# Performance work log

Hardware: AMD Instinct MI355X
Metric: run time of the kernel (lower is better)

## Reference

```python
import jax, jax.numpy as jnp
import numpy as np

H = 4      # SSM / attn heads (d_model/headdim = 256/64)
WIN = 4    # attention window over bands


def _ln(x, g, b):
    m = jnp.mean(x, -1, keepdims=True)
    v = jnp.mean((x - m) ** 2, -1, keepdims=True)
    return (x - m) * jax.lax.rsqrt(v + 1e-5) * g + b


def setup_inputs() -> dict:
    key = jax.random.key(0)
    ks = jax.random.split(key, 24)
    def rn(i, shape, s=0.05):
        return jax.random.normal(ks[i], shape, jnp.float32) * s
    B, T, K, D = 2, 256, 8, 256
    return {
        "z": rn(0, (B, T, K, D), 1.0),
        "ln1_g": jnp.ones((D,), jnp.float32), "ln1_b": jnp.zeros((D,), jnp.float32),
        "Wx": rn(1, (D, D)), "conv_w": rn(2, (D, 4), 0.3), "Wz": rn(3, (D, D)),
        "Wb": rn(4, (D, H * 128)), "Wc": rn(5, (D, H * 128)), "Wdt": rn(6, (D, H)),
        "dt_bias": rn(7, (H,), 0.5), "A_log": rn(8, (H,), 0.5), "theta": rn(9, (H,), 1.0),
        "D_skip": rn(10, (H,), 1.0), "mimo_U": rn(11, (H, H), 0.5), "mimo_V": rn(12, (H, H), 0.5),
        "Wout": rn(13, (D, D)),
        "ln2_g": jnp.ones((D,), jnp.float32), "ln2_b": jnp.zeros((D,), jnp.float32),
        "attn_in_w": rn(14, (3 * D, D)), "attn_in_b": rn(15, (3 * D,), 0.02),
        "attn_out_w": rn(16, (D, D)), "attn_out_b": jnp.zeros((D,), jnp.float32),
        "ln3_g": jnp.ones((D,), jnp.float32), "ln3_b": jnp.zeros((D,), jnp.float32),
        "Wg": rn(17, (D, 4 * D)), "Wu": rn(18, (D, 4 * D)), "Wd": rn(19, (4 * D, D)),
    }


def _forward(z, ln1_g, ln1_b, Wx, conv_w, Wz, Wb, Wc, Wdt, dt_bias, A_log, theta,
             D_skip, mimo_U, mimo_V, Wout, ln2_g, ln2_b, attn_in_w, attn_in_b,
             attn_out_w, attn_out_b, ln3_g, ln3_b, Wg, Wu, Wd):
    B, T, K, D = z.shape
    P = D // H
    N = Wb.shape[1] // H
    # ---------- (a) intra-band Mamba3 (complex MIMO selective scan) ----------
    u = _ln(z, ln1_g, ln1_b)
    u = jnp.transpose(u, (0, 2, 1, 3)).reshape(B * K, T, D)   # [BK,T,D]
    x = u @ Wx
    # causal depthwise conv1d, kernel 4
    xp = jnp.pad(x, ((0, 0), (3, 0), (0, 0)))
    x = sum(xp[:, k:k + T, :] * conv_w[:, k] for k in range(4))
    x = jax.nn.silu(x)
    xh = x.reshape(B * K, T, H, P)
    Bm = (u @ Wb).reshape(B * K, T, H, N)
    Cm = (u @ Wc).reshape(B * K, T, H, N)
    Mmix = mimo_U @ mimo_V.T                                  # rank-r cross-head coupling
    Bm = jnp.einsum('hg,btgn->bthn', Mmix, Bm)
    dt = jax.nn.softplus(u @ Wdt + dt_bias)                   # [BK,T,H]
    A = -jnp.exp(A_log)                                       # stable real decay
    mag = jnp.exp(dt * A)
    ph = dt * theta                                           # harmonic rotation
    ar, ai = mag * jnp.cos(ph), mag * jnp.sin(ph)
    xs = tuple(jnp.moveaxis(t, 1, 0) for t in (xh, Bm, Cm, dt, ar, ai))
    h0 = jnp.zeros((B * K, H, N, P), x.dtype)

    def step(carry, s):
        h_re, h_im = carry
        xt, bt, ct, dtt, art, ait = s
        dBx = (dtt[:, :, None, None] * bt[:, :, :, None]) * xt[:, :, None, :]
        nr = art[:, :, None, None] * h_re - ait[:, :, None, None] * h_im + dBx
        ni = art[:, :, None, None] * h_im + ait[:, :, None, None] * h_re
        return (nr, ni), jnp.einsum('bhn,bhnp->bhp', ct, nr)   # Re(C . h)

    _, ys = jax.lax.scan(step, (h0, h0), xs)                  # ys: [T,BK,H,P]
    y = jnp.moveaxis(ys, 0, 1) + D_skip[None, None, :, None] * xh
    y = y.reshape(B * K, T, D) * jax.nn.silu(u @ Wz)
    y = y @ Wout
    z = z + jnp.transpose(y.reshape(B, K, T, D), (0, 2, 1, 3))
    # ---------- (b) inter-band windowed attention ----------
    zn = _ln(z, ln2_g, ln2_b).reshape(B * T, K, D)
    qkv = zn @ attn_in_w.T + attn_in_b
    q, k_, v = jnp.split(qkv, 3, axis=-1)
    hd = D // H
    def hs(t):
        return t.reshape(B * T, K // WIN, WIN, H, hd).transpose(0, 1, 3, 2, 4)
    q, k_, v = hs(q), hs(k_), hs(v)
    s = jnp.einsum('mwhqd,mwhkd->mwhqk', q, k_) * jnp.float32(1.0 / np.sqrt(hd))
    a = jax.nn.softmax(s, axis=-1)
    o = jnp.einsum('mwhqk,mwhkd->mwhqd', a, v).transpose(0, 1, 3, 2, 4).reshape(B * T, K, D)
    z = z + (o @ attn_out_w.T + attn_out_b).reshape(B, T, K, D)
    # ---------- (c) SwiGLU FFN ----------
    zf = _ln(z, ln3_g, ln3_b)
    z = z + (jax.nn.silu(zf @ Wg) * (zf @ Wu)) @ Wd
    return z


def reference(z, ln1_g, ln1_b, Wx, conv_w, Wz, Wb, Wc, Wdt, dt_bias, A_log, theta,
              D_skip, mimo_U, mimo_V, Wout, ln2_g, ln2_b, attn_in_w, attn_in_b,
              attn_out_w, attn_out_b, ln3_g, ln3_b, Wg, Wu, Wd):
    return _forward(z, ln1_g, ln1_b, Wx, conv_w, Wz, Wb, Wc, Wdt, dt_bias, A_log,
                    theta, D_skip, mimo_U, mimo_V, Wout, ln2_g, ln2_b, attn_in_w,
                    attn_in_b, attn_out_w, attn_out_b, ln3_g, ln3_b, Wg, Wu, Wd)
```

## Files before the change

kernel.cpp:

```cpp
#include <hip/hip_runtime.h>
#include <hip/hip_bf16.h>
#include <math.h>

typedef __hip_bfloat16 bf16;
typedef __attribute__((ext_vector_type(8))) short s16x8;
typedef __attribute__((ext_vector_type(4))) float f32x4;

__device__ __forceinline__ float siluf(float x) { return x / (1.f + __expf(-x)); }
__device__ __forceinline__ float bits2f(unsigned short u) {
    union { float f; unsigned i; } v; v.i = ((unsigned)u) << 16; return v.f;
}
__device__ __forceinline__ unsigned short f2bits(float f) {
    return (unsigned short)__bfloat16_as_ushort(__float2bfloat16(f));
}

#define KFL 1024
#define OFF_UB   (768*KFL)
#define OFF_DTV  (1280*KFL)
#define OFF_BMB  (1344*KFL)
#define OFF_CMB  (2368*KFL)
#define OFF_ZGB  (3392*KFL)
#define OFF_XB   (3904*KFL)
#define OFF_X2T  (4928*KFL)
#define OFF_P    (5440*KFL)
#define OFF_YGB  (7488*KFL)
#define OFF_Z1   (8000*KFL)
#define OFF_ZNB  OFF_UB
#define OFF_QKV  OFF_BMB
#define OFF_OB   (2880*KFL)
#define OFF_Z2   OFF_P
#define OFF_ZFB  (6464*KFL)
#define OFF_GG   OFF_BMB

#define W_BCZX 0
#define W_OUT  393216
#define W_QKV  458752
#define W_AO   655360
#define W_GU   720896
#define W_D    1245184

__global__ __launch_bounds__(256) void prep_ln1_kernel(
    const float* __restrict__ Wx, const float* __restrict__ Wb,
    const float* __restrict__ Wc, const float* __restrict__ Wz,
    const float* __restrict__ Wo, const float* __restrict__ Wqkv,
    const float* __restrict__ Wao, const float* __restrict__ Wg,
    const float* __restrict__ Wu, const float* __restrict__ Wd,
    const float* __restrict__ U, const float* __restrict__ V,
    unsigned short* __restrict__ wout,
    const float* __restrict__ z, const float* __restrict__ g1,
    const float* __restrict__ b1, const float* __restrict__ Wdt,
    const float* __restrict__ dt_bias,
    unsigned short* __restrict__ u, float4* __restrict__ dtv4)
{
    __shared__ __align__(16) float smem[64 * 65];
    int blk = blockIdx.x;
    int tid = threadIdx.x;
    if (blk < 368) {
        if (blk >= 304) {
            int off = blk - 304;
            const float* src; int dst, base;
            if (off < 48) { src = Wqkv; dst = W_QKV; base = off * 4096; }
            else          { src = Wao;  dst = W_AO;  base = (off - 48) * 4096; }
            #pragma unroll
            for (int i = 0; i < 16; i++) {
                int idx = base + tid + i * 256;
                wout[dst + idx] = f2bits(src[idx]);
            }
            return;
        }
        float* lds = smem;
        const float* src; int srcN, n0, sc0, k0, dstoff, dstK, mix = 0, t;
        if (blk < 32)       { t = blk;       src = Wb; srcN = 512;  dstoff = W_BCZX; dstK = 256;
                              n0 = (t >> 2) * 64;        sc0 = 0; k0 = (t & 3) * 64; mix = 1; }
        else if (blk < 64)  { t = blk - 32;  src = Wc; srcN = 512;  dstoff = W_BCZX; dstK = 256;
                              n0 = 512 + (t >> 2) * 64;  sc0 = (t >> 2) * 64; k0 = (t & 3) * 64; }
        else if (blk < 80)  { t = blk - 64;  src = Wz; srcN = 256;  dstoff = W_BCZX; dstK = 256;
                              n0 = 1024 + (t >> 2) * 64; sc0 = (t >> 2) * 64; k0 = (t & 3) * 64; }
        else if (blk < 96)  { t = blk - 80;  src = Wx; srcN = 256;  dstoff = W_BCZX; dstK = 256;
                              n0 = 1280 + (t >> 2) * 64; sc0 = (t >> 2) * 64; k0 = (t & 3) * 64; }
        else if (blk < 112) { t = blk - 96;  src = Wo; srcN = 256;  dstoff = W_OUT;  dstK = 256;
                              n0 = (t >> 2) * 64;        sc0 = n0; k0 = (t & 3) * 64; }
        else if (blk < 176) { t = blk - 112; src = Wg; srcN = 1024; dstoff = W_GU;   dstK = 256;
                              n0 = (t >> 2) * 64;        sc0 = n0; k0 = (t & 3) * 64; }
        else if (blk < 240) { t = blk - 176; src = Wu; srcN = 1024; dstoff = W_GU;   dstK = 256;
                              n0 = 1024 + (t >> 2) * 64; sc0 = (t >> 2) * 64; k0 = (t & 3) * 64; }
        else                { t = blk - 240; src = Wd; srcN = 256;  dstoff = W_D;    dstK = 1024;
                              n0 = (t >> 4) * 64;        sc0 = n0; k0 = (t & 15) * 64; }
        if (mix) {
            int h = n0 >> 7, scol = n0 & 127;
            float mm[4];
            #pragma unroll
            for (int g = 0; g < 4; g++) {
                float s = 0.f;
                #pragma unroll
                for (int j = 0; j < 4; j++) s += U[h * 4 + j] * V[g * 4 + j];
                mm[g] = s;
            }
            #pragma unroll
            for (int i = 0; i < 16; i++) {
                int idx = tid + i * 256;
                int kk = idx >> 6, nn = idx & 63;
                const float* row = src + (size_t)(k0 + kk) * 512 + scol + nn;
                lds[kk * 65 + nn] = mm[0] * row[0] + mm[1] * row[128]
                                  + mm[2] * row[256] + mm[3] * row[384];
            }
        } else {
            #pragma unroll
            for (int i = 0; i < 16; i++) {
                int idx = tid + i * 256;
                int kk = idx >> 6, nn = idx & 63;
                lds[kk * 65 + nn] = src[(size_t)(k0 + kk) * srcN + sc0 + nn];
            }
        }
        __syncthreads();
        #pragma unroll
        for (int i = 0; i < 16; i++) {
            int idx = tid + i * 256;
            int nn = idx >> 6, kk = idx & 63;
            wout[dstoff + (size_t)(n0 + nn) * dstK + k0 + kk] = f2bits(lds[kk * 65 + nn]);
        }
        return;
    }
    int r = blk - 368;
    float* lds = smem;
    float* dts = smem + 4;
    int t = r & 255, bk = r >> 8;
    int b_ = bk >> 3, k = bk & 7;
    int srcr = ((b_ * 256 + t) * 8 + k) * 256;
    int d = tid;
    float x = z[srcr + d];
    float v = x;
    #pragma unroll
    for (int off = 32; off; off >>= 1) v += __shfl_xor(v, off, 64);
    if ((d & 63) == 0) lds[d >> 6] = v;
    __syncthreads();
    float mean = (lds[0] + lds[1] + lds[2] + lds[3]) * (1.f / 256.f);
    __syncthreads();
    float c = x - mean;
    v = c * c;
    #pragma unroll
    for (int off = 32; off; off >>= 1) v += __shfl_xor(v, off, 64);
    if ((d & 63) == 0) lds[d >> 6] = v;
    __syncthreads();
    float var = (lds[0] + lds[1] + lds[2] + lds[3]) * (1.f / 256.f);
    float uval = c * rsqrtf(var + 1e-5f) * g1[d] + b1[d];
    u[r * 256 + d] = f2bits(uval);
    float4 wv = *(const float4*)(Wdt + d * 4);
    float q0 = uval * wv.x, q1 = uval * wv.y, q2 = uval * wv.z, q3 = uval * wv.w;
    #pragma unroll
    for (int off = 32; off; off >>= 1) {
        q0 += __shfl_xor(q0, off, 64);
        q1 += __shfl_xor(q1, off, 64);
        q2 += __shfl_xor(q2, off, 64);
        q3 += __shfl_xor(q3, off, 64);
    }
    if ((d & 63) == 0) {
        int w = d >> 6;
        dts[w * 4 + 0] = q0; dts[w * 4 + 1] = q1;
        dts[w * 4 + 2] = q2; dts[w * 4 + 3] = q3;
    }
    __syncthreads();
    if (d == 0) {
        float dv[4];
        #pragma unroll
        for (int h = 0; h < 4; h++) {
            float xx = dts[h] + dts[4 + h] + dts[8 + h] + dts[12 + h] + dt_bias[h];
            dv[h] = (xx > 20.f) ? xx : log1pf(__expf(xx));
        }
        dtv4[r] = make_float4(dv[0], dv[1], dv[2], dv[3]);
    }
}

__global__ __launch_bounds__(256) void gemm_bczx(
    const unsigned short* __restrict__ A, const unsigned short* __restrict__ Bt,
    unsigned short* __restrict__ bmb, unsigned short* __restrict__ cmb,
    unsigned short* __restrict__ zgb, unsigned short* __restrict__ xb)
{
    __shared__ unsigned short As[128 * 40];
    __shared__ unsigned short Bs[128 * 40];
    const int K = 256;
    int tid = threadIdx.x;
    int n0 = blockIdx.x * 128, m0 = blockIdx.y * 128;
    int w = tid >> 6, l = tid & 63;
    int mwave = (w >> 1) * 64, nwave = (w & 1) * 64;
    f32x4 acc[4][4] = {};
    int srow = tid >> 2, sc = (tid & 3) * 8;
    const unsigned short* Ap = A + (size_t)(m0 + srow) * K + sc;
    const unsigned short* Bp = Bt + (size_t)(n0 + srow) * K + sc;
    int lq = l & 15, lh = l >> 4, ko = lh * 8;
    uint4 a0 = *(const uint4*)(Ap);
    uint4 a1 = *(const uint4*)(Ap + (size_t)64 * K);
    uint4 b0 = *(const uint4*)(Bp);
    uint4 b1 = *(const uint4*)(Bp + (size_t)64 * K);
    for (int k0 = 0; k0 < K; k0 += 32) {
        if (k0) __syncthreads();
        *(uint4*)&As[srow * 40 + sc] = a0;
        *(uint4*)&As[(srow + 64) * 40 + sc] = a1;
        *(uint4*)&Bs[srow * 40 + sc] = b0;
        *(uint4*)&Bs[(srow + 64) * 40 + sc] = b1;
        __syncthreads();
        if (k0 + 32 < K) {
            a0 = *(const uint4*)(Ap + k0 + 32);
            a1 = *(const uint4*)(Ap + (size_t)64 * K + k0 + 32);
            b0 = *(const uint4*)(Bp + k0 + 32);
            b1 = *(const uint4*)(Bp + (size_t)64 * K + k0 + 32);
        }
        s16x8 bfr[4];
        #pragma unroll
        for (int nf = 0; nf < 4; nf++)
            bfr[nf] = *(const s16x8*)&Bs[(nwave + nf * 16 + lq) * 40 + ko];
        #pragma unroll
        for (int mf = 0; mf < 4; mf++) {
            s16x8 af = *(const s16x8*)&As[(mwave + mf * 16 + lq) * 40 + ko];
            #pragma unroll
            for (int nf = 0; nf < 4; nf++)
                acc[mf][nf] = __builtin_amdgcn_mfma_f32_16x16x32_bf16(af, bfr[nf], acc[mf][nf], 0, 0, 0);
        }
    }
    #pragma unroll
    for (int mf = 0; mf < 4; mf++) {
        #pragma unroll
        for (int nf = 0; nf < 4; nf++) {
            int n = n0 + nwave + nf * 16 + lq;
            #pragma unroll
            for (int r = 0; r < 4; r++) {
                int m = m0 + mwave + mf * 16 + lh * 4 + r;
                float v = acc[mf][nf][r];
                if (n < 512)       bmb[(size_t)m * 512 + n] = f2bits(v);
                else if (n < 1024) cmb[(size_t)m * 512 + (n - 512)] = f2bits(v);
                else if (n < 1280) zgb[(size_t)m * 256 + (n - 1024)] = f2bits(siluf(v));
                else               xb[(size_t)m * 256 + (n - 1280)] = f2bits(v);
            }
        }
    }
}

__global__ __launch_bounds__(256) void s_conv_kernel(
    const unsigned short* __restrict__ cmb, const unsigned short* __restrict__ bmb,
    const float4* __restrict__ dtv4, const float* __restrict__ A_log,
    const float* __restrict__ theta, unsigned short* __restrict__ P,
    const unsigned short* __restrict__ xb, const float* __restrict__ cw,
    unsigned short* __restrict__ x2t)
{
    __shared__ __align__(16) char smem[23808];
    int blk = blockIdx.x;
    int tid = threadIdx.x;
    if (blk >= 192) {
        int c = blk - 192;
        int bhid = c >> 2, tt = c & 3;
        int bk = bhid >> 2, h = bhid & 3;
        int t0 = tt * 64;
        float* tile = (float*)smem;
        #pragma unroll
        for (int i = 0; i < 17; i++) {
            int idx = tid + i * 256;
            if (idx < 67 * 64) {
                int tr = idx >> 6, dd = idx & 63;
                int t = t0 - 3 + tr;
                tile[tr * 65 + dd] = (t >= 0)
                    ? bits2f(xb[(size_t)(bk * 256 + t) * 256 + h * 64 + dd]) : 0.f;
            }
        }
        __syncthreads();
        int wv_ = tid >> 6, lt = tid & 63;
        #pragma unroll 4
        for (int pi = 0; pi < 16; pi++) {
            int p = wv_ * 16 + pi;
            float4 wv = *(const float4*)(cw + (h * 64 + p) * 4);
            float acc = tile[lt * 65 + p] * wv.x + tile[(lt + 1) * 65 + p] * wv.y +
                        tile[(lt + 2) * 65 + p] * wv.z + tile[(lt + 3) * 65 + p] * wv.w;
            x2t[(size_t)(bhid * 64 + p) * 256 + t0 + lt] = f2bits(siluf(acc));
        }
        return;
    }
    int map = blk >> 6;
    int bh = blk & 63;
    int bx = (map == 2) ? 1 : 0;
    int by = (map == 0) ? 0 : 1;
    int bk = bh >> 2, h = bh & 3;
    unsigned short* As = (unsigned short*)smem;
    unsigned short* Bs = As + 128 * 40;
    float* mAs = (float*)(smem + 20480);
    float* phs = mAs + 256;
    float* dss = phs + 256;
    {
        float4 dv = dtv4[bk * 256 + tid];
        float dth = (h == 0) ? dv.x : (h == 1) ? dv.y : (h == 2) ? dv.z : dv.w;
        float Ah = -__expf(A_log[h]);
        float th = theta[h];
        dss[tid] = dth;
        mAs[tid] = dth * Ah;
        phs[tid] = dth * th;
        __syncthreads();
        for (int off = 1; off < 256; off <<= 1) {
            float a = 0.f, p = 0.f;
            int use = (tid >= off);
            if (use) { a = mAs[tid - off]; p = phs[tid - off]; }
            __syncthreads();
            if (use) { mAs[tid] += a; phs[tid] += p; }
            __syncthreads();
        }
    }
    int w = tid >> 6, l = tid & 63;
    int mwave = (w >> 1) * 64, nwave = (w & 1) * 64;
    int lq = l & 15, lh = l >> 4, ko = lh * 8;
    unsigned short* Pout = P + (size_t)bh * 65536;
    f32x4 acc[4][4] = {};
    int srow = tid >> 2, sc = (tid & 3) * 8;
    const unsigned short* Ap = cmb + (size_t)(bk * 256 + by * 128 + srow) * 512 + h * 128 + sc;
    const unsigned short* Bp = bmb + (size_t)(bk * 256 + bx * 128 + srow) * 512 + h * 128 + sc;
    uint4 a0 = *(const uint4*)(Ap);
    uint4 a1 = *(const uint4*)(Ap + (size_t)64 * 512);
    uint4 b0 = *(const uint4*)(Bp);
    uint4 b1 = *(const uint4*)(Bp + (size_t)64 * 512);
    for (int k0 = 0; k0 < 128; k0 += 32) {
        __syncthreads();
        *(uint4*)&As[srow * 40 + sc] = a0;
        *(uint4*)&As[(srow + 64) * 40 + sc] = a1;
        *(uint4*)&Bs[srow * 40 + sc] = b0;
        *(uint4*)&Bs[(srow + 64) * 40 + sc] = b1;
        __syncthreads();
        if (k0 + 32 < 128) {
            a0 = *(const uint4*)(Ap + k0 + 32);
            a1 = *(const uint4*)(Ap + (size_t)64 * 512 + k0 + 32);
            b0 = *(const uint4*)(Bp + k0 + 32);
            b1 = *(const uint4*)(Bp + (size_t)64 * 512 + k0 + 32);
        }
        s16x8 bfr[4];
        #pragma unroll
        for (int nf = 0; nf < 4; nf++)
            bfr[nf] = *(const s16x8*)&Bs[(nwave + nf * 16 + lq) * 40 + ko];
        #pragma unroll
        for (int mf = 0; mf < 4; mf++) {
            s16x8 af = *(const s16x8*)&As[(mwave + mf * 16 + lq) * 40 + ko];
            #pragma unroll
            for (int nf = 0; nf < 4; nf++)
                acc[mf][nf] = __builtin_amdgcn_mfma_f32_16x16x32_bf16(af, bfr[nf], acc[mf][nf], 0, 0, 0);
        }
    }
    #pragma unroll
    for (int mf = 0; mf < 4; mf++) {
        float tmv[4], tpv[4]; int tg[4];
        #pragma unroll
        for (int r = 0; r < 4; r++) {
            tg[r] = by * 128 + mwave + mf * 16 + lh * 4 + r;
            tmv[r] = mAs[tg[r]];
            tpv[r] = phs[tg[r]];
        }
        #pragma unroll
        for (int nf = 0; nf < 4; nf++) {
            int s = bx * 128 + nwave + nf * 16 + lq;
            float ms = mAs[s];
            float ps = phs[s];
            float ds = dss[s];
            #pragma unroll
            for (int r = 0; r < 4; r++) {
                float wgt = (s <= tg[r])
                    ? __expf(tmv[r] - ms) * __cosf(tpv[r] - ps) * ds : 0.f;
                Pout[tg[r] * 256 + s] = f2bits(acc[mf][nf][r] * wgt);
            }
        }
    }
}

__global__ __launch_bounds__(256) void gemm_y(
    const unsigned short* __restrict__ P, const unsigned short* __restrict__ x2t,
    const unsigned short* __restrict__ zgb, const float* __restrict__ Dsk,
    unsigned short* __restrict__ ygb)
{
    int by = blockIdx.x, bh = blockIdx.y;
    int bk = bh >> 2, h = bh & 3;
    int tid = threadIdx.x;
    int w = tid >> 6, l = tid & 63;
    int mw = (w >> 1) * 32, nw = (w & 1) * 32;
    int lq = l & 15, lh = l >> 4, ko = lh * 8;
    __shared__ unsigned short As[64 * 40];
    __shared__ unsigned short Bs[64 * 40];
    f32x4 acc[2][2] = {};
    int srow = tid >> 2, sc = (tid & 3) * 8;
    const unsigned short* Ap = P + (size_t)bh * 65536 + (size_t)(by * 64 + srow) * 256 + sc;
    const unsigned short* Bp = x2t + (size_t)bh * 16384 + (size_t)srow * 256 + sc;
    int kmax = (by + 1) * 64; if (kmax > 256) kmax = 256;
    uint4 a0 = *(const uint4*)(Ap);
    uint4 b0 = *(const uint4*)(Bp);
    for (int k0 = 0; k0 < kmax; k0 += 32) {
        if (k0) __syncthreads();
        *(uint4*)&As[srow * 40 + sc] = a0;
        *(uint4*)&Bs[srow * 40 + sc] = b0;
        __syncthreads();
        if (k0 + 32 < kmax) {
            a0 = *(const uint4*)(Ap + k0 + 32);
            b0 = *(const uint4*)(Bp + k0 + 32);
        }
        s16x8 bfr[2];
        #pragma unroll
        for (int nf = 0; nf < 2; nf++)
            bfr[nf] = *(const s16x8*)&Bs[(nw + nf * 16 + lq) * 40 + ko];
        #pragma unroll
        for (int mf = 0; mf < 2; mf++) {
            s16x8 af = *(const s16x8*)&As[(mw + mf * 16 + lq) * 40 + ko];
            #pragma unroll
            for (int nf = 0; nf < 2; nf++)
                acc[mf][nf] = __builtin_amdgcn_mfma_f32_16x16x32_bf16(af, bfr[nf], acc[mf][nf], 0, 0, 0);
        }
    }
    float dsk = Dsk[h];
    #pragma unroll
    for (int mf = 0; mf < 2; mf++) {
        #pragma unroll
        for (int nf = 0; nf < 2; nf++) {
            int p = nw + nf * 16 + lq;
            #pragma unroll
            for (int r = 0; r < 4; r++) {
                int t = by * 64 + mw + mf * 16 + lh * 4 + r;
                float xv = bits2f(x2t[(size_t)bh * 16384 + p * 256 + t]);
                float zg = bits2f(zgb[(size_t)(bk * 256 + t) * 256 + h * 64 + p]);
                ygb[(size_t)(bk * 256 + t) * 256 + h * 64 + p] =
                    f2bits((acc[mf][nf][r] + dsk * xv) * zg);
            }
        }
    }
}

__global__ __launch_bounds__(256) void gemm_ln(
    const unsigned short* __restrict__ A, const unsigned short* __restrict__ Bt,
    const float* __restrict__ bias, const float* __restrict__ resid,
    const float* __restrict__ g, const float* __restrict__ b,
    float* __restrict__ zfull, unsigned short* __restrict__ znorm, int rowmap)
{
    const int K = 256;
    __shared__ unsigned short As[16 * 40];
    __shared__ unsigned short Bs[256 * 40];
    __shared__ float partS[16][4], partQ[16][4];
    int tid = threadIdx.x;
    int m0 = blockIdx.x * 16;
    int w = tid >> 6, l = tid & 63;
    int nw = w * 64;
    int lq = l & 15, lh = l >> 4, ko = lh * 8;
    f32x4 acc[4] = {};
    int srow = tid >> 2, sc = (tid & 3) * 8;
    const unsigned short* Ap = A + (size_t)(m0 + (srow & 15)) * K + sc;
    const unsigned short* Bp = Bt + (size_t)srow * K + sc;
    uint4 a0 = *(const uint4*)(Ap);
    uint4 b0 = *(const uint4*)(Bp);
    uint4 b1 = *(const uint4*)(Bp + (size_t)64 * K);
    uint4 b2 = *(const uint4*)(Bp + (size_t)128 * K);
    uint4 b3 = *(const uint4*)(Bp + (size_t)192 * K);
    for (int k0 = 0; k0 < K; k0 += 32) {
        if (k0) __syncthreads();
        if (tid < 64) *(uint4*)&As[srow * 40 + sc] = a0;
        *(uint4*)&Bs[srow * 40 + sc] = b0;
        *(uint4*)&Bs[(srow + 64) * 40 + sc] = b1;
        *(uint4*)&Bs[(srow + 128) * 40 + sc] = b2;
        *(uint4*)&Bs[(srow + 192) * 40 + sc] = b3;
        __syncthreads();
        if (k0 + 32 < K) {
            a0 = *(const uint4*)(Ap + k0 + 32);
            b0 = *(const uint4*)(Bp + k0 + 32);
            b1 = *(const uint4*)(Bp + (size_t)64 * K + k0 + 32);
            b2 = *(const uint4*)(Bp + (size_t)128 * K + k0 + 32);
            b3 = *(const uint4*)(Bp + (size_t)192 * K + k0 + 32);
        }
        s16x8 af = *(const s16x8*)&As[lq * 40 + ko];
        #pragma unroll
        for (int nf = 0; nf < 4; nf++) {
            s16x8 bf = *(const s16x8*)&Bs[(nw + nf * 16 + lq) * 40 + ko];
            acc[nf] = __builtin_amdgcn_mfma_f32_16x16x32_bf16(af, bf, acc[nf], 0, 0, 0);
        }
    }
    float bv[4];
    #pragma unroll
    for (int nf = 0; nf < 4; nf++) bv[nf] = bias ? bias[nw + nf * 16 + lq] : 0.f;
    int orow[4];
    #pragma unroll
    for (int r = 0; r < 4; r++) {
        int rb = m0 + lh * 4 + r;
        if (rowmap) {
            int bk = rb >> 8, t = rb & 255;
            orow[r] = ((bk >> 3) * 256 + t) * 8 + (bk & 7);
        } else orow[r] = rb;
    }
    #pragma unroll
    for (int r = 0; r < 4; r++) {
        float s = 0.f, q = 0.f;
        #pragma unroll
        for (int nf = 0; nf < 4; nf++) {
            float v = acc[nf][r] + bv[nf]
                    + resid[(size_t)orow[r] * 256 + nw + nf * 16 + lq];
            acc[nf][r] = v;
            s += v; q += v * v;
        }
        #pragma unroll
        for (int off = 1; off < 16; off <<= 1) {
            s += __shfl_xor(s, off, 64);
            q += __shfl_xor(q, off, 64);
        }
        if (lq == 0) {
            int row = lh * 4 + r;
            partS[row][w] = s; partQ[row][w] = q;
        }
    }
    __syncthreads();
    float gv[4], bbv[4];
    #pragma unroll
    for (int nf = 0; nf < 4; nf++) {
        gv[nf] = g[nw + nf * 16 + lq];
        bbv[nf] = b[nw + nf * 16 + lq];
    }
    #pragma unroll
    for (int r = 0; r < 4; r++) {
        int row = lh * 4 + r;
        float sum = partS[row][0] + partS[row][1] + partS[row][2] + partS[row][3];
        float sq  = partQ[row][0] + partQ[row][1] + partQ[row][2] + partQ[row][3];
        float mean = sum * (1.f / 256.f);
        float var = sq * (1.f / 256.f) - mean * mean;
        float rstd = rsqrtf(var + 1e-5f);
        size_t ro = (size_t)orow[r] * 256;
        #pragma unroll
        for (int nf = 0; nf < 4; nf++) {
            int n = nw + nf * 16 + lq;
            float v = acc[nf][r];
            zfull[ro + n] = v;
            znorm[ro + n] = f2bits((v - mean) * rstd * gv[nf] + bbv[nf]);
        }
    }
}

__global__ __launch_bounds__(256) void mfma_gemm(
    const unsigned short* __restrict__ A, const unsigned short* __restrict__ Bt,
    const float* __restrict__ bias, void* __restrict__ C,
    int N, int K, int out_bf16)
{
    __shared__ unsigned short As[128 * 40];
    __shared__ unsigned short Bs[128 * 40];
    int tid = threadIdx.x;
    int n0 = blockIdx.x * 128, m0 = blockIdx.y * 128;
    int w = tid >> 6, l = tid & 63;
    int mwave = (w >> 1) * 64, nwave = (w & 1) * 64;
    f32x4 acc[4][4] = {};
    int srow = tid >> 2, sc = (tid & 3) * 8;
    const unsigned short* Ap = A + (size_t)(m0 + srow) * K + sc;
    const unsigned short* Bp = Bt + (size_t)(n0 + srow) * K + sc;
    int lq = l & 15, lh = l >> 4, ko = lh * 8;
    uint4 a0 = *(const uint4*)(Ap);
    uint4 a1 = *(const uint4*)(Ap + (size_t)64 * K);
    uint4 b0 = *(const uint4*)(Bp);
    uint4 b1 = *(const uint4*)(Bp + (size_t)64 * K);
    for (int k0 = 0; k0 < K; k0 += 32) {
        if (k0) __syncthreads();
        *(uint4*)&As[srow * 40 + sc] = a0;
        *(uint4*)&As[(srow + 64) * 40 + sc] = a1;
        *(uint4*)&Bs[srow * 40 + sc] = b0;
        *(uint4*)&Bs[(srow + 64) * 40 + sc] = b1;
        __syncthreads();
        if (k0 + 32 < K) {
            a0 = *(const uint4*)(Ap + k0 + 32);
            a1 = *(const uint4*)(Ap + (size_t)64 * K + k0 + 32);
            b0 = *(const uint4*)(Bp + k0 + 32);
            b1 = *(const uint4*)(Bp + (size_t)64 * K + k0 + 32);
        }
        s16x8 bfr[4];
        #pragma unroll
        for (int nf = 0; nf < 4; nf++)
            bfr[nf] = *(const s16x8*)&Bs[(nwave + nf * 16 + lq) * 40 + ko];
        #pragma unroll
        for (int mf = 0; mf < 4; mf++) {
            s16x8 af = *(const s16x8*)&As[(mwave + mf * 16 + lq) * 40 + ko];
            #pragma unroll
            for (int nf = 0; nf < 4; nf++)
                acc[mf][nf] = __builtin_amdgcn_mfma_f32_16x16x32_bf16(af, bfr[nf], acc[mf][nf], 0, 0, 0);
        }
    }
    #pragma unroll
    for (int mf = 0; mf < 4; mf++) {
        #pragma unroll
        for (int nf = 0; nf < 4; nf++) {
            int n = n0 + nwave + nf * 16 + lq;
            float bs_ = bias ? bias[n] : 0.f;
            #pragma unroll
            for (int r = 0; r < 4; r++) {
                int m = m0 + mwave + mf * 16 + lh * 4 + r;
                float v = acc[mf][nf][r] + bs_;
                if (out_bf16) ((unsigned short*)C)[(size_t)m * N + n] = f2bits(v);
                else          ((float*)C)[(size_t)m * N + n] = v;
            }
        }
    }
}

__global__ __launch_bounds__(256) void gemm_gu2(
    const unsigned short* __restrict__ A, const unsigned short* __restrict__ Wgu,
    unsigned short* __restrict__ gg)
{
    const int K = 256;
    __shared__ unsigned short As[128 * 40];
    __shared__ unsigned short Bgs[64 * 40];
    __shared__ unsigned short Bus[64 * 40];
    int tid = threadIdx.x;
    int n0 = blockIdx.x * 64, m0 = blockIdx.y * 128;
    int w = tid >> 6, l = tid & 63;
    int mwave = (w >> 1) * 64, nwave = (w & 1) * 32;
    int lq = l & 15, lh = l >> 4, ko = lh * 8;
    f32x4 ag[4][2] = {}, au[4][2] = {};
    int srow = tid >> 2, sc = (tid & 3) * 8;
    const unsigned short* Ap = A + (size_t)(m0 + srow) * K + sc;
    const unsigned short* Bgp = Wgu + (size_t)(n0 + srow) * K + sc;
    const unsigned short* Bup = Wgu + (size_t)(1024 + n0 + srow) * K + sc;
    uint4 a0 = *(const uint4*)(Ap);
    uint4 a1 = *(const uint4*)(Ap + (size_t)64 * K);
    uint4 bg = *(const uint4*)(Bgp);
    uint4 bu = *(const uint4*)(Bup);
    for (int k0 = 0; k0 < K; k0 += 32) {
        if (k0) __syncthreads();
        *(uint4*)&As[srow * 40 + sc] = a0;
        *(uint4*)&As[(srow + 64) * 40 + sc] = a1;
        *(uint4*)&Bgs[srow * 40 + sc] = bg;
        *(uint4*)&Bus[srow * 40 + sc] = bu;
        __syncthreads();
        if (k0 + 32 < K) {
            a0 = *(const uint4*)(Ap + k0 + 32);
            a1 = *(const uint4*)(Ap + (size_t)64 * K + k0 + 32);
            bg = *(const uint4*)(Bgp + k0 + 32);
            bu = *(const uint4*)(Bup + k0 + 32);
        }
        s16x8 bgr[2], bur[2];
        #pragma unroll
        for (int nf = 0; nf < 2; nf++) {
            bgr[nf] = *(const s16x8*)&Bgs[(nwave + nf * 16 + lq) * 40 + ko];
            bur[nf] = *(const s16x8*)&Bus[(nwave + nf * 16 + lq) * 40 + ko];
        }
        #pragma unroll
        for (int mf = 0; mf < 4; mf++) {
            s16x8 af = *(const s16x8*)&As[(mwave + mf * 16 + lq) * 40 + ko];
            #pragma unroll
            for (int nf = 0; nf < 2; nf++) {
                ag[mf][nf] = __builtin_amdgcn_mfma_f32_16x16x32_bf16(af, bgr[nf], ag[mf][nf], 0, 0, 0);
                au[mf][nf] = __builtin_amdgcn_mfma_f32_16x16x32_bf16(af, bur[nf], au[mf][nf], 0, 0, 0);
            }
        }
    }
    #pragma unroll
    for (int mf = 0; mf < 4; mf++) {
        #pragma unroll
        for (int nf = 0; nf < 2; nf++) {
            int n = n0 + nwave + nf * 16 + lq;
            #pragma unroll
            for (int r = 0; r < 4; r++) {
                int m = m0 + mwave + mf * 16 + lh * 4 + r;
                gg[(size_t)m * 1024 + n] = f2bits(siluf(ag[mf][nf][r]) * au[mf][nf][r]);
            }
        }
    }
}

__global__ __launch_bounds__(256) void gemm_d2(
    const unsigned short* __restrict__ gg, const unsigned short* __restrict__ Bt,
    const float* __restrict__ resid, float* __restrict__ out)
{
    __shared__ unsigned short As[64 * 40];
    __shared__ unsigned short Bs[64 * 40];
    const int K = 1024, N = 256;
    int tid = threadIdx.x;
    int n0 = blockIdx.x * 64, m0 = blockIdx.y * 64;
    int w = tid >> 6, l = tid & 63;
    int mw = (w >> 1) * 32, nw = (w & 1) * 32;
    f32x4 acc[2][2] = {};
    int srow = tid >> 2, sc = (tid & 3) * 8;
    const unsigned short* Ap = gg + (size_t)(m0 + srow) * K + sc;
    const unsigned short* Bp = Bt + (size_t)(n0 + srow) * K + sc;
    int lq = l & 15, lh = l >> 4, ko = lh * 8;
    uint4 a0 = *(const uint4*)(Ap);
    uint4 b0 = *(const uint4*)(Bp);
    for (int k0 = 0; k0 < K; k0 += 32) {
        if (k0) __syncthreads();
        *(uint4*)&As[srow * 40 + sc] = a0;
        *(uint4*)&Bs[srow * 40 + sc] = b0;
        __syncthreads();
        if (k0 + 32 < K) {
            a0 = *(const uint4*)(Ap + k0 + 32);
            b0 = *(const uint4*)(Bp + k0 + 32);
        }
        s16x8 bfr[2];
        #pragma unroll
        for (int nf = 0; nf < 2; nf++)
            bfr[nf] = *(const s16x8*)&Bs[(nw + nf * 16 + lq) * 40 + ko];
        #pragma unroll
        for (int mf = 0; mf < 2; mf++) {
            s16x8 af = *(const s16x8*)&As[(mw + mf * 16 + lq) * 40 + ko];
            #pragma unroll
            for (int nf = 0; nf < 2; nf++)
                acc[mf][nf] = __builtin_amdgcn_mfma_f32_16x16x32_bf16(af, bfr[nf], acc[mf][nf], 0, 0, 0);
        }
    }
    #pragma unroll
    for (int mf = 0; mf < 2; mf++) {
        #pragma unroll
        for (int nf = 0; nf < 2; nf++) {
            int n = n0 + nw + nf * 16 + lq;
            #pragma unroll
            for (int r = 0; r < 4; r++) {
                int m = m0 + mw + mf * 16 + lh * 4 + r;
                out[(size_t)m * N + n] = acc[mf][nf][r] + resid[(size_t)m * N + n];
            }
        }
    }
}

__global__ __launch_bounds__(256) void attn_kernel(const unsigned short* __restrict__ qkv,
    unsigned short* __restrict__ o)
{
    int m = blockIdx.x >> 1, w = blockIdx.x & 1;
    int tid = threadIdx.x;
    int h = tid >> 6, d = tid & 63;
    __shared__ float qs[4][256], ks[4][256], vs[4][256];
    #pragma unroll
    for (int j = 0; j < 4; j++) {
        int row = m * 8 + w * 4 + j;
        int base = row * 768;
        qs[j][tid] = bits2f(qkv[base + tid]);
        ks[j][tid] = bits2f(qkv[base + 256 + tid]);
        vs[j][tid] = bits2f(qkv[base + 512 + tid]);
    }
    __syncthreads();
    float sc[4][4];
    #pragma unroll
    for (int qi = 0; qi < 4; qi++)
        #pragma unroll
        for (int ki = 0; ki < 4; ki++) {
            float v = qs[qi][h * 64 + d] * ks[ki][h * 64 + d];
            #pragma unroll
            for (int off = 32; off; off >>= 1) v += __shfl_xor(v, off, 64);
            sc[qi][ki] = v * 0.125f;
        }
    #pragma unroll
    for (int qi = 0; qi < 4; qi++) {
        float mx = fmaxf(fmaxf(sc[qi][0], sc[qi][1]), fmaxf(sc[qi][2], sc[qi][3]));
        float e0 = __expf(sc[qi][0] - mx), e1 = __expf(sc[qi][1] - mx);
        float e2 = __expf(sc[qi][2] - mx), e3 = __expf(sc[qi][3] - mx);
        float inv = 1.f / (e0 + e1 + e2 + e3);
        float ov = (e0 * vs[0][h * 64 + d] + e1 * vs[1][h * 64 + d] +
                    e2 * vs[2][h * 64 + d] + e3 * vs[3][h * 64 + d]) * inv;
        o[(m * 8 + w * 4 + qi) * 256 + h * 64 + d] = f2bits(ov);
    }
}

extern "C" void kernel_launch(void* const* d_in, const int* in_sizes, int n_in,
                              void* d_out, int out_size, void* d_ws, size_t ws_size,
                              hipStream_t stream)
{
    const float* z         = (const float*)d_in[0];
    const float* ln1_g     = (const float*)d_in[1];
    const float* ln1_b     = (const float*)d_in[2];
    const float* Wx        = (const float*)d_in[3];
    const float* conv_w    = (const float*)d_in[4];
    const float* Wz        = (const float*)d_in[5];
    const float* Wb        = (const float*)d_in[6];
    const float* Wc        = (const float*)d_in[7];
    const float* Wdt       = (const float*)d_in[8];
    const float* dt_bias   = (const float*)d_in[9];
    const float* A_log     = (const float*)d_in[10];
    const float* theta     = (const float*)d_in[11];
    const float* D_skip    = (const float*)d_in[12];
    const float* mimo_U    = (const float*)d_in[13];
    const float* mimo_V    = (const float*)d_in[14];
    const float* Wout      = (const float*)d_in[15];
    const float* ln2_g     = (const float*)d_in[16];
    const float* ln2_b     = (const float*)d_in[17];
    const float* attn_in_w = (const float*)d_in[18];
    const float* attn_in_b = (const float*)d_in[19];
    const float* attn_out_w= (const float*)d_in[20];
    const float* attn_out_b= (const float*)d_in[21];
    const float* ln3_g     = (const float*)d_in[22];
    const float* ln3_b     = (const float*)d_in[23];
    const float* Wg        = (const float*)d_in[24];
    const float* Wu        = (const float*)d_in[25];
    const float* Wd        = (const float*)d_in[26];

    float* W = (float*)d_ws;
    unsigned short* wts = (unsigned short*)W;
    unsigned short* ub  = (unsigned short*)(W + OFF_UB);
    float4* dtv4        = (float4*)(W + OFF_DTV);
    unsigned short* bmb = (unsigned short*)(W + OFF_BMB);
    unsigned short* cmb = (unsigned short*)(W + OFF_CMB);
    unsigned short* zgb = (unsigned short*)(W + OFF_ZGB);
    unsigned short* xb  = (unsigned short*)(W + OFF_XB);
    unsigned short* x2t = (unsigned short*)(W + OFF_X2T);
    unsigned short* pbuf= (unsigned short*)(W + OFF_P);
    unsigned short* ygb = (unsigned short*)(W + OFF_YGB);
    float* z1           = W + OFF_Z1;
    unsigned short* znb = (unsigned short*)(W + OFF_ZNB);
    unsigned short* qkvb= (unsigned short*)(W + OFF_QKV);
    unsigned short* ob  = (unsigned short*)(W + OFF_OB);
    float* z2           = W + OFF_Z2;
    unsigned short* zfb = (unsigned short*)(W + OFF_ZFB);
    unsigned short* gg  = (unsigned short*)(W + OFF_GG);

    prep_ln1_kernel<<<4464, 256, 0, stream>>>(
        Wx, Wb, Wc, Wz, Wout, attn_in_w, attn_out_w, Wg, Wu, Wd, mimo_U, mimo_V,
        wts, z, ln1_g, ln1_b, Wdt, dt_bias, ub, dtv4);
    gemm_bczx<<<dim3(12, 32), 256, 0, stream>>>(ub, wts + W_BCZX, bmb, cmb, zgb, xb);
    s_conv_kernel<<<448, 256, 0, stream>>>(cmb, bmb, dtv4, A_log, theta, pbuf,
                                           xb, conv_w, x2t);
    gemm_y<<<dim3(4, 64), 256, 0, stream>>>(pbuf, x2t, zgb, D_skip, ygb);
    gemm_ln<<<256, 256, 0, stream>>>(ygb, wts + W_OUT, nullptr, z, ln2_g, ln2_b,
                                     z1, znb, 1);
    mfma_gemm<<<dim3(6, 32), 256, 0, stream>>>(znb, wts + W_QKV, attn_in_b, qkvb, 768, 256, 1);
    attn_kernel<<<1024, 256, 0, stream>>>(qkvb, ob);
    gemm_ln<<<256, 256, 0, stream>>>(ob, wts + W_AO, attn_out_b, z1, ln3_g, ln3_b,
                                     z2, zfb, 0);
    gemm_gu2<<<dim3(16, 32), 256, 0, stream>>>(zfb, wts + W_GU, gg);
    gemm_d2<<<dim3(4, 64), 256, 0, stream>>>(gg, wts + W_D, z2, (float*)d_out);
}
```

Measured before the change: 215.7 us.

## Move decay/phase prefix scan into gemm_bczx extra blocks; deepen K tiles to 64

The per-(batch-band) cumulative sums of dt*A and dt*theta are now computed once for all four heads, using float4 values in extra blocks of the gemm_bczx launch, and written to global buffers. s_conv_kernel reads these instead of each of its 192 blocks redoing a 256-step shared-memory scan with 16 barriers. Separately, gemm_y and gemm_d2 stage 64-wide K slices per iteration instead of 32, which halves the number of barrier pairs at the cost of more LDS per block. The extra scan blocks add a 13th column to the grid and write two new workspace regions. Those regions must not overlap other buffers.

```diff
diff --git a/kernel.cpp b/kernel.cpp
--- a/kernel.cpp
+++ b/kernel.cpp
@@ -17,6 +17,8 @@
 #define KFL 1024
 #define OFF_UB   (768*KFL)
 #define OFF_DTV  (1280*KFL)
+#define OFF_MAG  (1296*KFL)
+#define OFF_PHG  (1312*KFL)
 #define OFF_BMB  (1344*KFL)
 #define OFF_CMB  (2368*KFL)
 #define OFF_ZGB  (3392*KFL)
@@ -174,12 +176,44 @@
 __global__ __launch_bounds__(256) void gemm_bczx(
     const unsigned short* __restrict__ A, const unsigned short* __restrict__ Bt,
     unsigned short* __restrict__ bmb, unsigned short* __restrict__ cmb,
-    unsigned short* __restrict__ zgb, unsigned short* __restrict__ xb)
-{
-    __shared__ unsigned short As[128 * 40];
-    __shared__ unsigned short Bs[128 * 40];
+    unsigned short* __restrict__ zgb, unsigned short* __restrict__ xb,
+    const float4* __restrict__ dtv4, const float* __restrict__ A_log,
+    const float* __restrict__ theta, float4* __restrict__ mA4,
+    float4* __restrict__ ph4)
+{
+    __shared__ __align__(16) unsigned short As[128 * 40];
+    __shared__ __align__(16) unsigned short Bs[128 * 40];
     const int K = 256;
     int tid = threadIdx.x;
+    if (blockIdx.x == 12) {
+        int bk = blockIdx.y;
+        if (bk >= 16) return;
+        float4* s1 = (float4*)As;
+        float4* s2 = (float4*)Bs;
+        float4 dv = dtv4[bk * 256 + tid];
+        float A0 = -__expf(A_log[0]), A1 = -__expf(A_log[1]);
+        float A2 = -__expf(A_log[2]), A3 = -__expf(A_log[3]);
+        s1[tid] = make_float4(dv.x * A0, dv.y * A1, dv.z * A2, dv.w * A3);
+        s2[tid] = make_float4(dv.x * theta[0], dv.y * theta[1],
+                              dv.z * theta[2], dv.w * theta[3]);
+        __syncthreads();
+        for (int off = 1; off < 256; off <<= 1) {
+            float4 u1, u2;
+            int use = (tid >= off);
+            if (use) { u1 = s1[tid - off]; u2 = s2[tid - off]; }
+            __syncthreads();
+            if (use) {
+                float4 v1 = s1[tid], v2 = s2[tid];
+                v1.x += u1.x; v1.y += u1.y; v1.z += u1.z; v1.w += u1.w;
+                v2.x += u2.x; v2.y += u2.y; v2.z += u2.z; v2.w += u2.w;
+                s1[tid] = v1; s2[tid] = v2;
+            }
+            __syncthreads();
+        }
+        mA4[bk * 256 + tid] = s1[tid];
+        ph4[bk * 256 + tid] = s2[tid];
+        return;
+    }
     int n0 = blockIdx.x * 128, m0 = blockIdx.y * 128;
     int w = tid >> 6, l = tid & 63;
     int mwave = (w >> 1) * 64, nwave = (w & 1) * 64;
@@ -237,8 +271,8 @@
 
 __global__ __launch_bounds__(256) void s_conv_kernel(
     const unsigned short* __restrict__ cmb, const unsigned short* __restrict__ bmb,
-    const float4* __restrict__ dtv4, const float* __restrict__ A_log,
-    const float* __restrict__ theta, unsigned short* __restrict__ P,
+    const float4* __restrict__ dtv4, const float4* __restrict__ mA4,
+    const float4* __restrict__ ph4, unsigned short* __restrict__ P,
     const unsigned short* __restrict__ xb, const float* __restrict__ cw,
     unsigned short* __restrict__ x2t)
 {
@@ -285,21 +319,11 @@
     float* dss = phs + 256;
     {
         float4 dv = dtv4[bk * 256 + tid];
-        float dth = (h == 0) ? dv.x : (h == 1) ? dv.y : (h == 2) ? dv.z : dv.w;
-        float Ah = -__expf(A_log[h]);
-        float th = theta[h];
-        dss[tid] = dth;
-        mAs[tid] = dth * Ah;
-        phs[tid] = dth * th;
-        __syncthreads();
-        for (int off = 1; off < 256; off <<= 1) {
-            float a = 0.f, p = 0.f;
-            int use = (tid >= off);
-            if (use) { a = mAs[tid - off]; p = phs[tid - off]; }
-            __syncthreads();
-            if (use) { mAs[tid] += a; phs[tid] += p; }
-            __syncthreads();
-        }
+        float4 ma = mA4[bk * 256 + tid];
+        float4 pp = ph4[bk * 256 + tid];
+        dss[tid] = (h == 0) ? dv.x : (h == 1) ? dv.y : (h == 2) ? dv.z : dv.w;
+        mAs[tid] = (h == 0) ? ma.x : (h == 1) ? ma.y : (h == 2) ? ma.z : ma.w;
+        phs[tid] = (h == 0) ? pp.x : (h == 1) ? pp.y : (h == 2) ? pp.z : pp.w;
     }
     int w = tid >> 6, l = tid & 63;
     int mwave = (w >> 1) * 64, nwave = (w & 1) * 64;
@@ -374,34 +398,43 @@
     int w = tid >> 6, l = tid & 63;
     int mw = (w >> 1) * 32, nw = (w & 1) * 32;
     int lq = l & 15, lh = l >> 4, ko = lh * 8;
-    __shared__ unsigned short As[64 * 40];
-    __shared__ unsigned short Bs[64 * 40];
+    __shared__ unsigned short As[64 * 72];
+    __shared__ unsigned short Bs[64 * 72];
     f32x4 acc[2][2] = {};
     int srow = tid >> 2, sc = (tid & 3) * 8;
     const unsigned short* Ap = P + (size_t)bh * 65536 + (size_t)(by * 64 + srow) * 256 + sc;
     const unsigned short* Bp = x2t + (size_t)bh * 16384 + (size_t)srow * 256 + sc;
     int kmax = (by + 1) * 64; if (kmax > 256) kmax = 256;
     uint4 a0 = *(const uint4*)(Ap);
+    uint4 a1 = *(const uint4*)(Ap + 32);
     uint4 b0 = *(const uint4*)(Bp);
-    for (int k0 = 0; k0 < kmax; k0 += 32) {
+    uint4 b1 = *(const uint4*)(Bp + 32);
+    for (int k0 = 0; k0 < kmax; k0 += 64) {
         if (k0) __syncthreads();
-        *(uint4*)&As[srow * 40 + sc] = a0;
-        *(uint4*)&Bs[srow * 40 + sc] = b0;
-        __syncthreads();
-        if (k0 + 32 < kmax) {
-            a0 = *(const uint4*)(Ap + k0 + 32);
-            b0 = *(const uint4*)(Bp + k0 + 32);
-        }
-        s16x8 bfr[2];
-        #pragma unroll
-        for (int nf = 0; nf < 2; nf++)
-            bfr[nf] = *(const s16x8*)&Bs[(nw + nf * 16 + lq) * 40 + ko];
-        #pragma unroll
-        for (int mf = 0; mf < 2; mf++) {
-            s16x8 af = *(const s16x8*)&As[(mw + mf * 16 + lq) * 40 + ko];
+        *(uint4*)&As[srow * 72 + sc] = a0;
+        *(uint4*)&As[srow * 72 + sc + 32] = a1;
+        *(uint4*)&Bs[srow * 72 + sc] = b0;
+        *(uint4*)&Bs[srow * 72 + sc + 32] = b1;
+        __syncthreads();
+        if (k0 + 64 < kmax) {
+            a0 = *(const uint4*)(Ap + k0 + 64);
+            a1 = *(const uint4*)(Ap + k0 + 96);
+            b0 = *(const uint4*)(Bp + k0 + 64);
+            b1 = *(const uint4*)(Bp + k0 + 96);
+        }
+        #pragma unroll
+        for (int kk = 0; kk < 64; kk += 32) {
+            s16x8 bfr[2];
             #pragma unroll
             for (int nf = 0; nf < 2; nf++)
-                acc[mf][nf] = __builtin_amdgcn_mfma_f32_16x16x32_bf16(af, bfr[nf], acc[mf][nf], 0, 0, 0);
+                bfr[nf] = *(const s16x8*)&Bs[(nw + nf * 16 + lq) * 72 + kk + ko];
+            #pragma unroll
+            for (int mf = 0; mf < 2; mf++) {
+                s16x8 af = *(const s16x8*)&As[(mw + mf * 16 + lq) * 72 + kk + ko];
+                #pragma unroll
+                for (int nf = 0; nf < 2; nf++)
+                    acc[mf][nf] = __builtin_amdgcn_mfma_f32_16x16x32_bf16(af, bfr[nf], acc[mf][nf], 0, 0, 0);
+            }
         }
     }
     float dsk = Dsk[h];
@@ -657,8 +690,8 @@
     const unsigned short* __restrict__ gg, const unsigned short* __restrict__ Bt,
     const float* __restrict__ resid, float* __restrict__ out)
 {
-    __shared__ unsigned short As[64 * 40];
-    __shared__ unsigned short Bs[64 * 40];
+    __shared__ unsigned short As[64 * 72];
+    __shared__ unsigned short Bs[64 * 72];
     const int K = 1024, N = 256;
     int tid = threadIdx.x;
     int n0 = blockIdx.x * 64, m0 = blockIdx.y * 64;
@@ -670,26 +703,35 @@
     const unsigned short* Bp = Bt + (size_t)(n0 + srow) * K + sc;
     int lq = l & 15, lh = l >> 4, ko = lh * 8;
     uint4 a0 = *(const uint4*)(Ap);
+    uint4 a1 = *(const uint4*)(Ap + 32);
     uint4 b0 = *(const uint4*)(Bp);
-    for (int k0 = 0; k0 < K; k0 += 32) {
+    uint4 b1 = *(const uint4*)(Bp + 32);
+    for (int k0 = 0; k0 < K; k0 += 64) {
         if (k0) __syncthreads();
-        *(uint4*)&As[srow * 40 + sc] = a0;
-        *(uint4*)&Bs[srow * 40 + sc] = b0;
-        __syncthreads();
-        if (k0 + 32 < K) {
-            a0 = *(const uint4*)(Ap + k0 + 32);
-            b0 = *(const uint4*)(Bp + k0 + 32);
-        }
-        s16x8 bfr[2];
-        #pragma unroll
-        for (int nf = 0; nf < 2; nf++)
-            bfr[nf] = *(const s16x8*)&Bs[(nw + nf * 16 + lq) * 40 + ko];
-        #pragma unroll
-        for (int mf = 0; mf < 2; mf++) {
-            s16x8 af = *(const s16x8*)&As[(mw + mf * 16 + lq) * 40 + ko];
+        *(uint4*)&As[srow * 72 + sc] = a0;
+        *(uint4*)&As[srow * 72 + sc + 32] = a1;
+        *(uint4*)&Bs[srow * 72 + sc] = b0;
+        *(uint4*)&Bs[srow * 72 + sc + 32] = b1;
+        __syncthreads();
+        if (k0 + 64 < K) {
+            a0 = *(const uint4*)(Ap + k0 + 64);
+            a1 = *(const uint4*)(Ap + k0 + 96);
+            b0 = *(const uint4*)(Bp + k0 + 64);
+            b1 = *(const uint4*)(Bp + k0 + 96);
+        }
+        #pragma unroll
+        for (int kk = 0; kk < 64; kk += 32) {
+            s16x8 bfr[2];
             #pragma unroll
             for (int nf = 0; nf < 2; nf++)
-                acc[mf][nf] = __builtin_amdgcn_mfma_f32_16x16x32_bf16(af, bfr[nf], acc[mf][nf], 0, 0, 0);
+                bfr[nf] = *(const s16x8*)&Bs[(nw + nf * 16 + lq) * 72 + kk + ko];
+            #pragma unroll
+            for (int mf = 0; mf < 2; mf++) {
+                s16x8 af = *(const s16x8*)&As[(mw + mf * 16 + lq) * 72 + kk + ko];
+                #pragma unroll
+                for (int nf = 0; nf < 2; nf++)
+                    acc[mf][nf] = __builtin_amdgcn_mfma_f32_16x16x32_bf16(af, bfr[nf], acc[mf][nf], 0, 0, 0);
+            }
         }
     }
     #pragma unroll
@@ -780,6 +822,8 @@
     unsigned short* wts = (unsigned short*)W;
     unsigned short* ub  = (unsigned short*)(W + OFF_UB);
     float4* dtv4        = (float4*)(W + OFF_DTV);
+    float4* mA4g        = (float4*)(W + OFF_MAG);
+    float4* ph4g        = (float4*)(W + OFF_PHG);
     unsigned short* bmb = (unsigned short*)(W + OFF_BMB);
     unsigned short* cmb = (unsigned short*)(W + OFF_CMB);
     unsigned short* zgb = (unsigned short*)(W + OFF_ZGB);
@@ -798,8 +842,9 @@
     prep_ln1_kernel<<<4464, 256, 0, stream>>>(
         Wx, Wb, Wc, Wz, Wout, attn_in_w, attn_out_w, Wg, Wu, Wd, mimo_U, mimo_V,
         wts, z, ln1_g, ln1_b, Wdt, dt_bias, ub, dtv4);
-    gemm_bczx<<<dim3(12, 32), 256, 0, stream>>>(ub, wts + W_BCZX, bmb, cmb, zgb, xb);
-    s_conv_kernel<<<448, 256, 0, stream>>>(cmb, bmb, dtv4, A_log, theta, pbuf,
+    gemm_bczx<<<dim3(13, 32), 256, 0, stream>>>(ub, wts + W_BCZX, bmb, cmb, zgb, xb,
+                                                dtv4, A_log, theta, mA4g, ph4g);
+    s_conv_kernel<<<448, 256, 0, stream>>>(cmb, bmb, dtv4, mA4g, ph4g, pbuf,
                                            xb, conv_w, x2t);
     gemm_y<<<dim3(4, 64), 256, 0, stream>>>(pbuf, x2t, zgb, D_skip, ygb);
     gemm_ln<<<256, 256, 0, stream>>>(ygb, wts + W_OUT, nullptr, z, ln2_g, ln2_b,
```

Measured after the change: 214.2 us. Within noise of the previous version (-0.7%).
